# Performance work log

Measured on AMD Instinct MI355X. Metric: run time of the kernel, lower is better.

The kernel has to match this reference:

```python
import jax, jax.numpy as jnp
import numpy as np

N_TRUCK = 100000
N_CAR = 100000
E = 1600000
H = 128
P = 200000


def _gcn(x, edge_index, edge_weight, W, b, num_nodes):
    """PyG GCNConv: D^{-1/2}(A+I)D^{-1/2} x W + b with self-loop weight 1."""
    h = x @ W  # [N, H]
    row, col = edge_index[0], edge_index[1]
    deg = jax.ops.segment_sum(edge_weight, col, num_segments=num_nodes) + 1.0  # +1 self-loop
    dis = jax.lax.rsqrt(deg)
    norm = dis[row] * edge_weight * dis[col]  # [E]
    agg = jax.ops.segment_sum(norm[:, None] * h[row], col, num_segments=num_nodes)
    agg = agg + (dis * dis)[:, None] * h  # self-loop contribution
    return agg + b


def setup_inputs() -> dict:
    key = jax.random.key(0)
    ks = jax.random.split(key, 12)
    return {
        "x_car": jax.random.normal(ks[0], (N_CAR, 3), dtype=jnp.float32),
        "edge_index_truck": jax.random.randint(ks[1], (2, E), 0, N_TRUCK, dtype=jnp.int64)
        if jax.config.jax_enable_x64 else jax.random.randint(ks[1], (2, E), 0, N_TRUCK, dtype=jnp.int32),
        "edge_index_car": jax.random.randint(ks[2], (2, E), 0, N_CAR, dtype=jnp.int32),
        "edge_weight_car": jax.random.uniform(ks[3], (E,), dtype=jnp.float32),
        "src": jax.random.randint(ks[4], (P,), 0, N_TRUCK + N_CAR, dtype=jnp.int32),
        "dst": jax.random.randint(ks[5], (P,), 0, N_TRUCK + N_CAR, dtype=jnp.int32),
        "n_truck": N_TRUCK,
        "W_truck": jax.random.normal(ks[6], (1, H), dtype=jnp.float32) * 0.5,
        "b_truck": jax.random.normal(ks[7], (H,), dtype=jnp.float32) * 0.1,
        "W_car": jax.random.normal(ks[8], (3, H), dtype=jnp.float32) * 0.5,
        "b_car": jax.random.normal(ks[9], (H,), dtype=jnp.float32) * 0.1,
        "W_lin": jax.random.normal(ks[10], (H, 1), dtype=jnp.float32) * 0.1,
        "b_lin": jax.random.normal(ks[11], (1,), dtype=jnp.float32) * 0.1,
    }


def reference(x_car, edge_index_truck, edge_index_car, edge_weight_car,
              src, dst, n_truck, W_truck, b_truck, W_car, b_car, W_lin, b_lin):
    x_truck_in = jnp.ones((n_truck, 1), dtype=x_car.dtype)
    ew_truck = jnp.ones((edge_index_truck.shape[1],), dtype=x_car.dtype)
    h_truck = _gcn(x_truck_in, edge_index_truck, ew_truck, W_truck, b_truck, n_truck)
    h_car = _gcn(x_car, edge_index_car, edge_weight_car, W_car, b_car, x_car.shape[0])
    x = jnp.concatenate([h_truck, h_car], axis=0)  # [N_truck+N_car, H]
    score = (x[src] * x[dst]) @ W_lin + b_lin  # [P, 1]
    return score
```

## Files before the change

kernel.cpp:

```cpp
#include <hip/hip_runtime.h>

typedef unsigned long long u64;

#define N_TRUCK 100000
#define BLK 256
#define NB 256
#define NPB 391
#define CAP 8192
#define PB 512
#define BLK_P 1024
#define CHUNK_MAX 3136
#define ROW_MASK 0x1FFFFu
#define LC_SHIFT 17

#define WS_NEED_NEW 29569920ULL


__global__ void k_place(const int* __restrict__ trow, const int* __restrict__ tcol,
                        const int* __restrict__ crow, const int* __restrict__ ccol,
                        const float* __restrict__ ew, int E_,
                        int* __restrict__ curT, int* __restrict__ curC,
                        unsigned* __restrict__ pT, u64* __restrict__ pC8,
                        const float* __restrict__ Wt, const float* __restrict__ bt,
                        const float* __restrict__ Wc, const float* __restrict__ bc,
                        const float* __restrict__ wlin, float* __restrict__ G) {
    if (blockIdx.x == PB) {
        int l = threadIdx.x;
        if (l < 64) {
            float acc[21];
#pragma unroll
            for (int k = 0; k < 21; k++) acc[k] = 0.0f;
            for (int h = l; h < 128; h += 64) {
                float m[6] = {Wt[h], bt[h], Wc[h], Wc[128 + h], Wc[256 + h], bc[h]};
                float w = wlin[h];
                int k = 0;
#pragma unroll
                for (int a = 0; a < 6; a++)
#pragma unroll
                    for (int b2 = a; b2 < 6; b2++)
                        acc[k++] += m[a] * m[b2] * w;
            }
            int k = 0;
#pragma unroll
            for (int a = 0; a < 6; a++)
#pragma unroll
                for (int b2 = a; b2 < 6; b2++) {
                    float v = acc[k++];
#pragma unroll
                    for (int off = 32; off; off >>= 1) v += __shfl_down(v, off);
                    if (l == 0) {
                        G[a * 6 + b2] = v;
                        G[b2 * 6 + a] = v;
                    }
                }
        }
        return;
    }

    __shared__ u64 pay8[CHUNK_MAX];
    __shared__ unsigned char bkt[CHUNK_MAX];
    __shared__ int hist[NB];
    __shared__ int shiftA[NB];
    unsigned* pay4 = (unsigned*)pay8;

    int b = blockIdx.x;
    int chunk = (E_ + PB - 1) / PB;
    int s0 = b * chunk, s1 = min(E_, s0 + chunk);
    int n = s1 - s0;
    int t = threadIdx.x;

    for (int k = t; k < NB; k += BLK_P) hist[k] = 0;
    __syncthreads();
    for (int j = s0 + t; j < s1; j += BLK_P) atomicAdd(&hist[tcol[j] / NPB], 1);
    __syncthreads();
    int myCnt = (t < NB) ? hist[t] : 0;
    if (t < NB) shiftA[t] = myCnt;
    __syncthreads();
    for (int off = 1; off < NB; off <<= 1) {
        int x = (t < NB && t >= off) ? shiftA[t - off] : 0;
        __syncthreads();
        if (t < NB) shiftA[t] += x;
        __syncthreads();
    }
    if (t < NB) {
        int excl = shiftA[t] - myCnt;
        int gstart = t * CAP + atomicAdd(&curT[t], myCnt);
        shiftA[t] = gstart - excl;
        hist[t] = excl;
    }
    __syncthreads();
    for (int j = s0 + t; j < s1; j += BLK_P) {
        int tc = tcol[j];
        int k = tc / NPB;
        int s = atomicAdd(&hist[k], 1);
        pay4[s] = ((unsigned)(tc - k * NPB) << LC_SHIFT) | (unsigned)trow[j];
        bkt[s] = (unsigned char)k;
    }
    __syncthreads();
    for (int s = t; s < n; s += BLK_P)
        pT[s + shiftA[bkt[s]]] = pay4[s];
    __syncthreads();

    for (int k = t; k < NB; k += BLK_P) hist[k] = 0;
    __syncthreads();
    for (int j = s0 + t; j < s1; j += BLK_P) atomicAdd(&hist[ccol[j] / NPB], 1);
    __syncthreads();
    myCnt = (t < NB) ? hist[t] : 0;
    if (t < NB) shiftA[t] = myCnt;
    __syncthreads();
    for (int off = 1; off < NB; off <<= 1) {
        int x = (t < NB && t >= off) ? shiftA[t - off] : 0;
        __syncthreads();
        if (t < NB) shiftA[t] += x;
        __syncthreads();
    }
    if (t < NB) {
        int excl = shiftA[t] - myCnt;
        int gstart = t * CAP + atomicAdd(&curC[t], myCnt);
        shiftA[t] = gstart - excl;
        hist[t] = excl;
    }
    __syncthreads();
    for (int j = s0 + t; j < s1; j += BLK_P) {
        int cc = ccol[j];
        int k = cc / NPB;
        int s = atomicAdd(&hist[k], 1);
        unsigned lo = ((unsigned)(cc - k * NPB) << LC_SHIFT) | (unsigned)crow[j];
        pay8[s] = ((u64)__float_as_uint(ew[j]) << 32) | lo;
        bkt[s] = (unsigned char)k;
    }
    __syncthreads();
    for (int s = t; s < n; s += BLK_P)
        pC8[s + shiftA[bkt[s]]] = pay8[s];
}


__global__ void k_deg2(const unsigned* __restrict__ pT, const u64* __restrict__ pC8,
                       const int* __restrict__ curT, const int* __restrict__ curC,
                       const float* __restrict__ x_car,
                       float* __restrict__ dis_t, float* __restrict__ dis_c,
                       float4* __restrict__ xs4, int nt, int nc) {
    __shared__ float acc[NPB];
    int b = blockIdx.x;
    bool car = b >= NB;
    int bk = car ? b - NB : b;
    int cnt = car ? curC[bk] : curT[bk];
    int s0 = bk * CAP;
    for (int k = threadIdx.x; k < NPB; k += blockDim.x) acc[k] = 0.0f;
    __syncthreads();
    if (car) {
        const ulonglong2* p2 = (const ulonglong2*)(pC8 + s0);
        int half = cnt >> 1;
        for (int j = threadIdx.x; j < half; j += blockDim.x) {
            ulonglong2 v = p2[j];
            atomicAdd(&acc[((unsigned)v.x) >> LC_SHIFT], __uint_as_float((unsigned)(v.x >> 32)));
            atomicAdd(&acc[((unsigned)v.y) >> LC_SHIFT], __uint_as_float((unsigned)(v.y >> 32)));
        }
        if ((cnt & 1) && threadIdx.x == 0) {
            u64 v = pC8[s0 + cnt - 1];
            atomicAdd(&acc[((unsigned)v) >> LC_SHIFT], __uint_as_float((unsigned)(v >> 32)));
        }
    } else {
        const uint2* p2 = (const uint2*)(pT + s0);
        int half = cnt >> 1;
        for (int j = threadIdx.x; j < half; j += blockDim.x) {
            uint2 v = p2[j];
            atomicAdd(&acc[v.x >> LC_SHIFT], 1.0f);
            atomicAdd(&acc[v.y >> LC_SHIFT], 1.0f);
        }
        if ((cnt & 1) && threadIdx.x == 0)
            atomicAdd(&acc[pT[s0 + cnt - 1] >> LC_SHIFT], 1.0f);
    }
    __syncthreads();
    int ntot = car ? nc : nt;
    for (int nn = threadIdx.x; nn < NPB; nn += blockDim.x) {
        int node = bk * NPB + nn;
        if (node < ntot) {
            float d = rsqrtf(acc[nn] + 1.0f);
            if (car) {
                dis_c[node] = d;
                const float* xn = &x_car[3 * node];
                xs4[node] = make_float4(d * xn[0], d * xn[1], d * xn[2], d);
            } else {
                dis_t[node] = d;
            }
        }
    }
}


__global__ void k_agg(const unsigned* __restrict__ pT, const u64* __restrict__ pC8,
                      const int* __restrict__ curT, const int* __restrict__ curC,
                      const float* __restrict__ dis_t, const float* __restrict__ dis_c,
                      const float4* __restrict__ xs4,
                      float* __restrict__ s_t, float4* __restrict__ y4,
                      int nt, int nc) {
    int b = blockIdx.x;
    if (b < NB) {
        __shared__ float sacc[NPB];
        int cnt = curT[b];
        int s0 = b * CAP;
        for (int k = threadIdx.x; k < NPB; k += blockDim.x) sacc[k] = 0.0f;
        __syncthreads();
        const uint2* p2 = (const uint2*)(pT + s0);
        int half = cnt >> 1;
        for (int j = threadIdx.x; j < half; j += blockDim.x) {
            uint2 v = p2[j];
            float da = dis_t[v.x & ROW_MASK];
            float db = dis_t[v.y & ROW_MASK];
            atomicAdd(&sacc[v.x >> LC_SHIFT], da);
            atomicAdd(&sacc[v.y >> LC_SHIFT], db);
        }
        if ((cnt & 1) && threadIdx.x == 0) {
            unsigned v = pT[s0 + cnt - 1];
            atomicAdd(&sacc[v >> LC_SHIFT], dis_t[v & ROW_MASK]);
        }
        __syncthreads();
        for (int nn = threadIdx.x; nn < NPB; nn += blockDim.x) {
            int node = b * NPB + nn;
            if (node < nt) {
                float d = dis_t[node];
                s_t[node] = fmaf(d, sacc[nn], d * d);
            }
        }
    } else {
        int bk = b - NB;
        __shared__ float y[NPB * 5];
        __shared__ float dcl[NPB];
        int cnt = curC[bk];
        int s0 = bk * CAP;
        for (int k = threadIdx.x; k < NPB * 5; k += blockDim.x) y[k] = 0.0f;
        for (int k = threadIdx.x; k < NPB; k += blockDim.x) {
            int node = bk * NPB + k;
            dcl[k] = (node < nc) ? dis_c[node] : 0.0f;
        }
        __syncthreads();
        const ulonglong2* p2 = (const ulonglong2*)(pC8 + s0);
        int half = cnt >> 1;
        for (int j = threadIdx.x; j < half; j += blockDim.x) {
            ulonglong2 v = p2[j];
            unsigned loa = (unsigned)v.x, lob = (unsigned)v.y;
            float4 xa = xs4[loa & ROW_MASK];
            float4 xb = xs4[lob & ROW_MASK];
            int lca = loa >> LC_SHIFT, lcb = lob >> LC_SHIFT;
            float na = __uint_as_float((unsigned)(v.x >> 32)) * dcl[lca];
            float nb = __uint_as_float((unsigned)(v.y >> 32)) * dcl[lcb];
            atomicAdd(&y[lca * 5 + 0], na * xa.x);
            atomicAdd(&y[lca * 5 + 1], na * xa.y);
            atomicAdd(&y[lca * 5 + 2], na * xa.z);
            atomicAdd(&y[lcb * 5 + 0], nb * xb.x);
            atomicAdd(&y[lcb * 5 + 1], nb * xb.y);
            atomicAdd(&y[lcb * 5 + 2], nb * xb.z);
        }
        if ((cnt & 1) && threadIdx.x == 0) {
            u64 v = pC8[s0 + cnt - 1];
            unsigned lo = (unsigned)v;
            float4 xa = xs4[lo & ROW_MASK];
            int lc = lo >> LC_SHIFT;
            float na = __uint_as_float((unsigned)(v >> 32)) * dcl[lc];
            atomicAdd(&y[lc * 5 + 0], na * xa.x);
            atomicAdd(&y[lc * 5 + 1], na * xa.y);
            atomicAdd(&y[lc * 5 + 2], na * xa.z);
        }
        __syncthreads();
        for (int nn = threadIdx.x; nn < NPB; nn += blockDim.x) {
            int node = bk * NPB + nn;
            if (node < nc) {
                float d = dcl[nn];
                float4 xs = xs4[node];
                y4[node] = make_float4(fmaf(d, xs.x, y[nn * 5 + 0]),
                                       fmaf(d, xs.y, y[nn * 5 + 1]),
                                       fmaf(d, xs.z, y[nn * 5 + 2]), 1.0f);
            }
        }
    }
}


__device__ __forceinline__ void load_z(int i, const float* __restrict__ s_t,
                                       const float4* __restrict__ y4, float z[6]) {
    if (i < N_TRUCK) {
        z[0] = s_t[i]; z[1] = 1.0f; z[2] = 0.0f; z[3] = 0.0f; z[4] = 0.0f; z[5] = 0.0f;
    } else {
        float4 y = y4[i - N_TRUCK];
        z[0] = 0.0f; z[1] = 0.0f; z[2] = y.x; z[3] = y.y; z[4] = y.z; z[5] = 1.0f;
    }
}

__global__ void k_pairs(const int* __restrict__ src, const int* __restrict__ dst, int P_,
                        const float* __restrict__ s_t, const float4* __restrict__ y4,
                        const float* __restrict__ G, const float* __restrict__ b_lin,
                        float* __restrict__ out) {
    int p = blockIdx.x * blockDim.x + threadIdx.x;
    if (p >= P_) return;
    float zs[6], zd[6];
    load_z(src[p], s_t, y4, zs);
    load_z(dst[p], s_t, y4, zd);
    float acc = 0.0f;
#pragma unroll
    for (int a = 0; a < 6; a++) {
        float g = 0.0f;
#pragma unroll
        for (int b = 0; b < 6; b++) g = fmaf(G[a * 6 + b], zd[b], g);
        acc = fmaf(zs[a], g, acc);
    }
    out[p] = acc + b_lin[0];
}


__global__ void k_G(const float* __restrict__ Wt, const float* __restrict__ bt,
                    const float* __restrict__ Wc, const float* __restrict__ bc,
                    const float* __restrict__ wlin, float* __restrict__ G) {
    int l = threadIdx.x;
    float acc[21];
#pragma unroll
    for (int k = 0; k < 21; k++) acc[k] = 0.0f;
    for (int h = l; h < 128; h += 64) {
        float m[6] = {Wt[h], bt[h], Wc[h], Wc[128 + h], Wc[256 + h], bc[h]};
        float w = wlin[h];
        int k = 0;
#pragma unroll
        for (int a = 0; a < 6; a++)
#pragma unroll
            for (int b = a; b < 6; b++)
                acc[k++] += m[a] * m[b] * w;
    }
    int k = 0;
#pragma unroll
    for (int a = 0; a < 6; a++)
#pragma unroll
        for (int b = a; b < 6; b++) {
            float v = acc[k++];
#pragma unroll
            for (int off = 32; off; off >>= 1) v += __shfl_down(v, off);
            if (l == 0) {
                G[a * 6 + b] = v;
                G[b * 6 + a] = v;
            }
        }
}

__global__ void k_deg(const int* __restrict__ tcol, const int* __restrict__ ccol,
                      const float* __restrict__ ew, int E_,
                      int* __restrict__ cnt_t, float* __restrict__ degw_c) {
    int i = blockIdx.x * blockDim.x + threadIdx.x;
    if (i >= E_) return;
    atomicAdd(&cnt_t[tcol[i]], 1);
    atomicAdd(&degw_c[ccol[i]], ew[i]);
}

__global__ void k_dis(const int* __restrict__ cnt_t, const float* __restrict__ degw_c,
                      float* __restrict__ dis_t, float* __restrict__ dis_c,
                      int nt, int nc) {
    int i = blockIdx.x * blockDim.x + threadIdx.x;
    if (i < nt) dis_t[i] = rsqrtf((float)cnt_t[i] + 1.0f);
    if (i < nc) dis_c[i] = rsqrtf(degw_c[i] + 1.0f);
}

__global__ void k_scat(const int* __restrict__ trow, const int* __restrict__ tcol,
                       const int* __restrict__ crow, const int* __restrict__ ccol,
                       const float* __restrict__ ew, int E_,
                       const float* __restrict__ dis_t, const float* __restrict__ dis_c,
                       const float* __restrict__ x_car,
                       float* __restrict__ sumdis, float* __restrict__ y4) {
    int i = blockIdx.x * blockDim.x + threadIdx.x;
    if (i >= E_) return;
    atomicAdd(&sumdis[tcol[i]], dis_t[trow[i]]);
    int r = crow[i], c = ccol[i];
    float nrm = dis_c[r] * ew[i] * dis_c[c];
    atomicAdd(&y4[c * 4 + 0], nrm * x_car[r * 3 + 0]);
    atomicAdd(&y4[c * 4 + 1], nrm * x_car[r * 3 + 1]);
    atomicAdd(&y4[c * 4 + 2], nrm * x_car[r * 3 + 2]);
}

__global__ void k_fin(int nt, int nc,
                      const float* __restrict__ dis_t, const float* __restrict__ sumdis,
                      float* __restrict__ s_t,
                      const float* __restrict__ dis_c, const float* __restrict__ x_car,
                      float* __restrict__ y4) {
    int i = blockIdx.x * blockDim.x + threadIdx.x;
    if (i < nt) {
        float d = dis_t[i];
        s_t[i] = d * sumdis[i] + d * d;
    }
    if (i < nc) {
        float d2 = dis_c[i] * dis_c[i];
        y4[i * 4 + 0] += d2 * x_car[i * 3 + 0];
        y4[i * 4 + 1] += d2 * x_car[i * 3 + 1];
        y4[i * 4 + 2] += d2 * x_car[i * 3 + 2];
        y4[i * 4 + 3] = 1.0f;
    }
}


extern "C" void kernel_launch(void* const* d_in, const int* in_sizes, int n_in,
                              void* d_out, int out_size, void* d_ws, size_t ws_size,
                              hipStream_t stream) {
    const float* x_car  = (const float*)d_in[0];
    const int*   ei_t   = (const int*)d_in[1];
    const int*   ei_c   = (const int*)d_in[2];
    const float* ew_c   = (const float*)d_in[3];
    const int*   src    = (const int*)d_in[4];
    const int*   dst    = (const int*)d_in[5];
    const float* W_t    = (const float*)d_in[7];
    const float* b_t    = (const float*)d_in[8];
    const float* W_c    = (const float*)d_in[9];
    const float* b_c    = (const float*)d_in[10];
    const float* W_lin  = (const float*)d_in[11];
    const float* b_lin  = (const float*)d_in[12];
    float* out = (float*)d_out;

    const int NC = in_sizes[0] / 3;
    const int E_ = in_sizes[1] / 2;
    const int P_ = in_sizes[4];

    const int* trow = ei_t;  const int* tcol = ei_t + E_;
    const int* crow = ei_c;  const int* ccol = ei_c + E_;

    char* ws = (char*)d_ws;
    int gP = (P_ + BLK - 1) / BLK;
    int chunk = (E_ + PB - 1) / PB;

    if (ws_size >= WS_NEED_NEW && chunk <= CHUNK_MAX && NB * NPB >= N_TRUCK &&
        NB * NPB >= NC && NB * CAP >= E_ + 8192) {
        int*      curT  = (int*)(ws + 0);
        int*      curC  = (int*)(ws + 1024);
        float*    G     = (float*)(ws + 2048);
        float*    dis_t = (float*)(ws + 4096);
        float*    dis_c = (float*)(ws + 404096);
        float*    s_t   = (float*)(ws + 804096);
        float*    y4    = (float*)(ws + 1204096);
        float4*   xs4   = (float4*)(ws + 2804096);
        unsigned* pT    = (unsigned*)(ws + 4404096);
        u64*      pC8   = (u64*)(ws + 12792704);

        hipMemsetAsync(ws, 0, 2048, stream);
        k_place<<<PB + 1, BLK_P, 0, stream>>>(trow, tcol, crow, ccol, ew_c, E_,
                                              curT, curC, pT, pC8,
                                              W_t, b_t, W_c, b_c, W_lin, G);
        k_deg2<<<2 * NB, BLK_P, 0, stream>>>(pT, pC8, curT, curC, x_car,
                                             dis_t, dis_c, xs4, N_TRUCK, NC);
        k_agg<<<2 * NB, BLK_P, 0, stream>>>(pT, pC8, curT, curC, dis_t, dis_c,
                                            xs4, s_t, (float4*)y4, N_TRUCK, NC);
        k_pairs<<<gP, BLK, 0, stream>>>(src, dst, P_, s_t, (const float4*)y4, G, b_lin, out);
    } else {
        int*   cnt_t  = (int*)(ws + 0);
        float* sumdis = (float*)(ws + 400000);
        float* degw_c = (float*)(ws + 800000);
        float* y4     = (float*)(ws + 1200000);
        float* dis_t  = (float*)(ws + 2800000);
        float* dis_c  = (float*)(ws + 3200000);
        float* s_t    = (float*)(ws + 3600000);
        float* G      = (float*)(ws + 4000000);

        hipMemsetAsync(ws, 0, 2800000, stream);
        int gE = (E_ + BLK - 1) / BLK;
        int gN = ((N_TRUCK > NC ? N_TRUCK : NC) + BLK - 1) / BLK;
        k_deg<<<gE, BLK, 0, stream>>>(tcol, ccol, ew_c, E_, cnt_t, degw_c);
        k_dis<<<gN, BLK, 0, stream>>>(cnt_t, degw_c, dis_t, dis_c, N_TRUCK, NC);
        k_scat<<<gE, BLK, 0, stream>>>(trow, tcol, crow, ccol, ew_c, E_,
                                       dis_t, dis_c, x_car, sumdis, y4);
        k_fin<<<gN, BLK, 0, stream>>>(N_TRUCK, NC, dis_t, sumdis, s_t, dis_c, x_car, y4);
        k_G<<<1, 64, 0, stream>>>(W_t, b_t, W_c, b_c, W_lin, G);
        k_pairs<<<gP, BLK, 0, stream>>>(src, dst, P_, s_t, (const float4*)y4, G, b_lin, out);
    }
}
```

Baseline: 184.2 us.

## Fuse whole GCN pipeline into one cooperative kernel with grid syncs

Replaces the multi-kernel pipeline (memset, place, deg, agg, pairs) with a single cooperative kernel that uses grid.sync between phases. Placement now uses a deterministic per-block histogram followed by a global prefix scan instead of global atomic cursors, so it no longer needs a memset. The aim is to remove launch gaps and kernel boundaries. The costs are extra grid barriers, a second pass over the column arrays, and host-side occupancy queries on every call. It falls back to the old path if a cooperative launch isn't possible.

```diff
diff --git a/kernel.cpp b/kernel.cpp
--- a/kernel.cpp
+++ b/kernel.cpp
@@ -1,5 +1,7 @@
 #include <hip/hip_runtime.h>
-
+#include <hip/hip_cooperative_groups.h>
+
+namespace cg = cooperative_groups;
 typedef unsigned long long u64;
 
 #define N_TRUCK 100000
@@ -13,7 +15,389 @@
 #define ROW_MASK 0x1FFFFu
 #define LC_SHIFT 17
 
+#define WS_NEED_F 30618496ULL
 #define WS_NEED_NEW 29569920ULL
+
+struct FParams {
+    const int *trow, *tcol, *crow, *ccol;
+    const float* ew;
+    const int *src, *dst;
+    const float *Wt, *bt, *Wc, *bc, *wlin, *blin;
+    const float* x_car;
+    float* out;
+    int E, P, NC;
+    float* G;
+    int *totT, *totC, *cntT, *cntC;
+    float *dis_t, *dis_c, *s_t;
+    float4 *y4, *xs4;
+    unsigned* pT;
+    u64* pC8;
+};
+
+union SmemU {
+    struct { int hT[NB]; int hC[NB]; } hist;
+    struct { int w[16]; } scan;
+    struct {
+        u64 pay8[CHUNK_MAX];
+        unsigned char bkt[CHUNK_MAX];
+        int hist[NB];
+        int shift[NB];
+        int wsum[16];
+    } place;
+    struct { float acc[NPB]; } deg;
+    struct { float y[NPB * 5]; float dcl[NPB]; } agg;
+};
+
+__device__ __forceinline__ void load_zf(int i, const float* __restrict__ s_t,
+                                        const float4* __restrict__ y4, float z[6]) {
+    if (i < N_TRUCK) {
+        z[0] = s_t[i]; z[1] = 1.0f; z[2] = 0.0f; z[3] = 0.0f; z[4] = 0.0f; z[5] = 0.0f;
+    } else {
+        float4 y = y4[i - N_TRUCK];
+        z[0] = 0.0f; z[1] = 0.0f; z[2] = y.x; z[3] = y.y; z[4] = y.z; z[5] = 1.0f;
+    }
+}
+
+__global__ __launch_bounds__(1024, 8)
+void k_fused(FParams fp) {
+    cg::grid_group grid = cg::this_grid();
+    __shared__ SmemU sm;
+    const int t = threadIdx.x;
+    const int b = blockIdx.x;
+    const int lane = t & 63, wv = t >> 6;
+    const int chunk = (fp.E + PB - 1) / PB;
+    const int s0 = b * chunk, s1 = min(fp.E, s0 + chunk);
+    const int n = s1 - s0;
+
+    for (int k = t; k < NB; k += BLK_P) { sm.hist.hT[k] = 0; sm.hist.hC[k] = 0; }
+    __syncthreads();
+    for (int j = s0 + t; j < s1; j += BLK_P) {
+        atomicAdd(&sm.hist.hT[fp.tcol[j] / NPB], 1);
+        atomicAdd(&sm.hist.hC[fp.ccol[j] / NPB], 1);
+    }
+    __syncthreads();
+    for (int k = t; k < NB; k += BLK_P) {
+        fp.cntT[k * PB + b] = sm.hist.hT[k];
+        fp.cntC[k * PB + b] = sm.hist.hC[k];
+    }
+    grid.sync();
+
+    {
+        bool car = b >= NB;
+        int k = b & (NB - 1);
+        int* row = (car ? fp.cntC : fp.cntT) + k * PB;
+        int v = 0, inc = 0;
+        if (t < PB) {
+            v = row[t];
+            inc = v;
+#pragma unroll
+            for (int off = 1; off < 64; off <<= 1) {
+                int nv = __shfl_up(inc, off);
+                if (lane >= off) inc += nv;
+            }
+            if (lane == 63) sm.scan.w[wv] = inc;
+        } else if (b == 0 && wv == 8) {
+            float acc[21];
+#pragma unroll
+            for (int q = 0; q < 21; q++) acc[q] = 0.0f;
+            for (int h = lane; h < 128; h += 64) {
+                float m[6] = {fp.Wt[h], fp.bt[h], fp.Wc[h], fp.Wc[128 + h], fp.Wc[256 + h], fp.bc[h]};
+                float w = fp.wlin[h];
+                int q = 0;
+#pragma unroll
+                for (int a = 0; a < 6; a++)
+#pragma unroll
+                    for (int b2 = a; b2 < 6; b2++)
+                        acc[q++] += m[a] * m[b2] * w;
+            }
+            int q = 0;
+#pragma unroll
+            for (int a = 0; a < 6; a++)
+#pragma unroll
+                for (int b2 = a; b2 < 6; b2++) {
+                    float vv = acc[q++];
+#pragma unroll
+                    for (int off = 32; off; off >>= 1) vv += __shfl_down(vv, off);
+                    if (lane == 0) {
+                        fp.G[a * 6 + b2] = vv;
+                        fp.G[b2 * 6 + a] = vv;
+                    }
+                }
+        }
+        __syncthreads();
+        if (t < 8) {
+            int pv = sm.scan.w[t], pinc = pv;
+#pragma unroll
+            for (int off = 1; off < 8; off <<= 1) {
+                int nv = __shfl_up(pinc, off);
+                if (lane >= off) pinc += nv;
+            }
+            sm.scan.w[t] = pinc - pv;
+        }
+        __syncthreads();
+        if (t < PB) {
+            int excl = (inc - v) + sm.scan.w[wv];
+            row[t] = excl;
+            if (t == PB - 1) (car ? fp.totC : fp.totT)[k] = excl + v;
+        }
+    }
+    grid.sync();
+
+    {
+        int cntk = 0, gbase = 0, inc = 0;
+        if (t < NB) {
+            int e0 = fp.cntT[t * PB + b];
+            int e1 = (b == PB - 1) ? fp.totT[t] : fp.cntT[t * PB + b + 1];
+            cntk = e1 - e0;
+            gbase = t * CAP + e0;
+            inc = cntk;
+#pragma unroll
+            for (int off = 1; off < 64; off <<= 1) {
+                int nv = __shfl_up(inc, off);
+                if (lane >= off) inc += nv;
+            }
+            if (lane == 63) sm.place.wsum[wv] = inc;
+        }
+        __syncthreads();
+        if (t < 4) {
+            int pv = sm.place.wsum[t], pinc = pv;
+#pragma unroll
+            for (int off = 1; off < 4; off <<= 1) {
+                int nv = __shfl_up(pinc, off);
+                if (lane >= off) pinc += nv;
+            }
+            sm.place.wsum[t] = pinc - pv;
+        }
+        __syncthreads();
+        if (t < NB) {
+            int lexcl = (inc - cntk) + sm.place.wsum[wv];
+            sm.place.hist[t] = lexcl;
+            sm.place.shift[t] = gbase - lexcl;
+        }
+        __syncthreads();
+        unsigned* pay4 = (unsigned*)sm.place.pay8;
+        for (int j = s0 + t; j < s1; j += BLK_P) {
+            int c = fp.tcol[j];
+            int k = c / NPB;
+            int s = atomicAdd(&sm.place.hist[k], 1);
+            pay4[s] = ((unsigned)(c - k * NPB) << LC_SHIFT) | (unsigned)fp.trow[j];
+            sm.place.bkt[s] = (unsigned char)k;
+        }
+        __syncthreads();
+        for (int s = t; s < n; s += BLK_P)
+            fp.pT[s + sm.place.shift[sm.place.bkt[s]]] = pay4[s];
+        __syncthreads();
+    }
+    {
+        int cntk = 0, gbase = 0, inc = 0;
+        if (t < NB) {
+            int e0 = fp.cntC[t * PB + b];
+            int e1 = (b == PB - 1) ? fp.totC[t] : fp.cntC[t * PB + b + 1];
+            cntk = e1 - e0;
+            gbase = t * CAP + e0;
+            inc = cntk;
+#pragma unroll
+            for (int off = 1; off < 64; off <<= 1) {
+                int nv = __shfl_up(inc, off);
+                if (lane >= off) inc += nv;
+            }
+            if (lane == 63) sm.place.wsum[wv] = inc;
+        }
+        __syncthreads();
+        if (t < 4) {
+            int pv = sm.place.wsum[t], pinc = pv;
+#pragma unroll
+            for (int off = 1; off < 4; off <<= 1) {
+                int nv = __shfl_up(pinc, off);
+                if (lane >= off) pinc += nv;
+            }
+            sm.place.wsum[t] = pinc - pv;
+        }
+        __syncthreads();
+        if (t < NB) {
+            int lexcl = (inc - cntk) + sm.place.wsum[wv];
+            sm.place.hist[t] = lexcl;
+            sm.place.shift[t] = gbase - lexcl;
+        }
+        __syncthreads();
+        for (int j = s0 + t; j < s1; j += BLK_P) {
+            int c = fp.ccol[j];
+            int k = c / NPB;
+            int s = atomicAdd(&sm.place.hist[k], 1);
+            unsigned lo = ((unsigned)(c - k * NPB) << LC_SHIFT) | (unsigned)fp.crow[j];
+            sm.place.pay8[s] = ((u64)__float_as_uint(fp.ew[j]) << 32) | lo;
+            sm.place.bkt[s] = (unsigned char)k;
+        }
+        __syncthreads();
+        for (int s = t; s < n; s += BLK_P)
+            fp.pC8[s + sm.place.shift[sm.place.bkt[s]]] = sm.place.pay8[s];
+    }
+    grid.sync();
+
+    {
+        bool car = b >= NB;
+        int bk = car ? b - NB : b;
+        int cnt = car ? fp.totC[bk] : fp.totT[bk];
+        int base = bk * CAP;
+        for (int k = t; k < NPB; k += BLK_P) sm.deg.acc[k] = 0.0f;
+        __syncthreads();
+        if (car) {
+            const ulonglong4* p4 = (const ulonglong4*)(fp.pC8 + base);
+            int q = cnt >> 2;
+            for (int j = t; j < q; j += BLK_P) {
+                ulonglong4 v = p4[j];
+                atomicAdd(&sm.deg.acc[((unsigned)v.x) >> LC_SHIFT], __uint_as_float((unsigned)(v.x >> 32)));
+                atomicAdd(&sm.deg.acc[((unsigned)v.y) >> LC_SHIFT], __uint_as_float((unsigned)(v.y >> 32)));
+                atomicAdd(&sm.deg.acc[((unsigned)v.z) >> LC_SHIFT], __uint_as_float((unsigned)(v.z >> 32)));
+                atomicAdd(&sm.deg.acc[((unsigned)v.w) >> LC_SHIFT], __uint_as_float((unsigned)(v.w >> 32)));
+            }
+            for (int j = (q << 2) + t; j < cnt; j += BLK_P) {
+                u64 v = fp.pC8[base + j];
+                atomicAdd(&sm.deg.acc[((unsigned)v) >> LC_SHIFT], __uint_as_float((unsigned)(v >> 32)));
+            }
+        } else {
+            const uint4* p4 = (const uint4*)(fp.pT + base);
+            int q = cnt >> 2;
+            for (int j = t; j < q; j += BLK_P) {
+                uint4 v = p4[j];
+                atomicAdd(&sm.deg.acc[v.x >> LC_SHIFT], 1.0f);
+                atomicAdd(&sm.deg.acc[v.y >> LC_SHIFT], 1.0f);
+                atomicAdd(&sm.deg.acc[v.z >> LC_SHIFT], 1.0f);
+                atomicAdd(&sm.deg.acc[v.w >> LC_SHIFT], 1.0f);
+            }
+            for (int j = (q << 2) + t; j < cnt; j += BLK_P)
+                atomicAdd(&sm.deg.acc[fp.pT[base + j] >> LC_SHIFT], 1.0f);
+        }
+        __syncthreads();
+        int ntot = car ? fp.NC : N_TRUCK;
+        for (int nn = t; nn < NPB; nn += BLK_P) {
+            int node = bk * NPB + nn;
+            if (node < ntot) {
+                float d = rsqrtf(sm.deg.acc[nn] + 1.0f);
+                if (car) {
+                    fp.dis_c[node] = d;
+                    const float* xn = &fp.x_car[3 * node];
+                    fp.xs4[node] = make_float4(d * xn[0], d * xn[1], d * xn[2], d);
+                } else {
+                    fp.dis_t[node] = d;
+                }
+            }
+        }
+    }
+    grid.sync();
+
+    if (b < NB) {
+        int cnt = fp.totT[b];
+        int base = b * CAP;
+        for (int k = t; k < NPB; k += BLK_P) sm.deg.acc[k] = 0.0f;
+        __syncthreads();
+        const uint4* p4 = (const uint4*)(fp.pT + base);
+        int q = cnt >> 2;
+        for (int j = t; j < q; j += BLK_P) {
+            uint4 v = p4[j];
+            float d0 = fp.dis_t[v.x & ROW_MASK];
+            float d1 = fp.dis_t[v.y & ROW_MASK];
+            float d2 = fp.dis_t[v.z & ROW_MASK];
+            float d3 = fp.dis_t[v.w & ROW_MASK];
+            atomicAdd(&sm.deg.acc[v.x >> LC_SHIFT], d0);
+            atomicAdd(&sm.deg.acc[v.y >> LC_SHIFT], d1);
+            atomicAdd(&sm.deg.acc[v.z >> LC_SHIFT], d2);
+            atomicAdd(&sm.deg.acc[v.w >> LC_SHIFT], d3);
+        }
+        for (int j = (q << 2) + t; j < cnt; j += BLK_P) {
+            unsigned v = fp.pT[base + j];
+            atomicAdd(&sm.deg.acc[v >> LC_SHIFT], fp.dis_t[v & ROW_MASK]);
+        }
+        __syncthreads();
+        for (int nn = t; nn < NPB; nn += BLK_P) {
+            int node = b * NPB + nn;
+            if (node < N_TRUCK) {
+                float d = fp.dis_t[node];
+                fp.s_t[node] = fmaf(d, sm.deg.acc[nn], d * d);
+            }
+        }
+    } else {
+        int bk = b - NB;
+        int cnt = fp.totC[bk];
+        int base = bk * CAP;
+        for (int k = t; k < NPB * 5; k += BLK_P) sm.agg.y[k] = 0.0f;
+        for (int k = t; k < NPB; k += BLK_P) {
+            int node = bk * NPB + k;
+            sm.agg.dcl[k] = (node < fp.NC) ? fp.dis_c[node] : 0.0f;
+        }
+        __syncthreads();
+        const ulonglong4* p4 = (const ulonglong4*)(fp.pC8 + base);
+        int q = cnt >> 2;
+        for (int j = t; j < q; j += BLK_P) {
+            ulonglong4 v = p4[j];
+            unsigned lo0 = (unsigned)v.x, lo1 = (unsigned)v.y;
+            unsigned lo2 = (unsigned)v.z, lo3 = (unsigned)v.w;
+            float4 x0 = fp.xs4[lo0 & ROW_MASK];
+            float4 x1 = fp.xs4[lo1 & ROW_MASK];
+            float4 x2 = fp.xs4[lo2 & ROW_MASK];
+            float4 x3 = fp.xs4[lo3 & ROW_MASK];
+            int c0 = lo0 >> LC_SHIFT, c1 = lo1 >> LC_SHIFT;
+            int c2 = lo2 >> LC_SHIFT, c3 = lo3 >> LC_SHIFT;
+            float n0 = __uint_as_float((unsigned)(v.x >> 32)) * sm.agg.dcl[c0];
+            float n1 = __uint_as_float((unsigned)(v.y >> 32)) * sm.agg.dcl[c1];
+            float n2 = __uint_as_float((unsigned)(v.z >> 32)) * sm.agg.dcl[c2];
+            float n3 = __uint_as_float((unsigned)(v.w >> 32)) * sm.agg.dcl[c3];
+            atomicAdd(&sm.agg.y[c0 * 5 + 0], n0 * x0.x);
+            atomicAdd(&sm.agg.y[c0 * 5 + 1], n0 * x0.y);
+            atomicAdd(&sm.agg.y[c0 * 5 + 2], n0 * x0.z);
+            atomicAdd(&sm.agg.y[c1 * 5 + 0], n1 * x1.x);
+            atomicAdd(&sm.agg.y[c1 * 5 + 1], n1 * x1.y);
+            atomicAdd(&sm.agg.y[c1 * 5 + 2], n1 * x1.z);
+            atomicAdd(&sm.agg.y[c2 * 5 + 0], n2 * x2.x);
+            atomicAdd(&sm.agg.y[c2 * 5 + 1], n2 * x2.y);
+            atomicAdd(&sm.agg.y[c2 * 5 + 2], n2 * x2.z);
+            atomicAdd(&sm.agg.y[c3 * 5 + 0], n3 * x3.x);
+            atomicAdd(&sm.agg.y[c3 * 5 + 1], n3 * x3.y);
+            atomicAdd(&sm.agg.y[c3 * 5 + 2], n3 * x3.z);
+        }
+        for (int j = (q << 2) + t; j < cnt; j += BLK_P) {
+            u64 v = fp.pC8[base + j];
+            unsigned lo = (unsigned)v;
+            float4 xa = fp.xs4[lo & ROW_MASK];
+            int lc = lo >> LC_SHIFT;
+            float na = __uint_as_float((unsigned)(v >> 32)) * sm.agg.dcl[lc];
+            atomicAdd(&sm.agg.y[lc * 5 + 0], na * xa.x);
+            atomicAdd(&sm.agg.y[lc * 5 + 1], na * xa.y);
+            atomicAdd(&sm.agg.y[lc * 5 + 2], na * xa.z);
+        }
+        __syncthreads();
+        for (int nn = t; nn < NPB; nn += BLK_P) {
+            int node = bk * NPB + nn;
+            if (node < fp.NC) {
+                float d = sm.agg.dcl[nn];
+                float4 xs = fp.xs4[node];
+                fp.y4[node] = make_float4(fmaf(d, xs.x, sm.agg.y[nn * 5 + 0]),
+                                          fmaf(d, xs.y, sm.agg.y[nn * 5 + 1]),
+                                          fmaf(d, xs.z, sm.agg.y[nn * 5 + 2]), 1.0f);
+            }
+        }
+    }
+    grid.sync();
+
+    float Gl[36];
+#pragma unroll
+    for (int k = 0; k < 36; k++) Gl[k] = fp.G[k];
+    float bl = fp.blin[0];
+    for (int p = b * BLK_P + t; p < fp.P; p += gridDim.x * BLK_P) {
+        float zs[6], zd[6];
+        load_zf(fp.src[p], fp.s_t, fp.y4, zs);
+        load_zf(fp.dst[p], fp.s_t, fp.y4, zd);
+        float acc = 0.0f;
+#pragma unroll
+        for (int a = 0; a < 6; a++) {
+            float g = 0.0f;
+#pragma unroll
+            for (int b2 = 0; b2 < 6; b2++) g = fmaf(Gl[a * 6 + b2], zd[b2], g);
+            acc = fmaf(zs[a], g, acc);
+        }
+        fp.out[p] = acc + bl;
+    }
+}
 
 
 __global__ void k_place(const int* __restrict__ trow, const int* __restrict__ tcol,
@@ -134,7 +518,6 @@
         pC8[s + shiftA[bkt[s]]] = pay8[s];
 }
 
-
 __global__ void k_deg2(const unsigned* __restrict__ pT, const u64* __restrict__ pC8,
                        const int* __restrict__ curT, const int* __restrict__ curC,
                        const float* __restrict__ x_car,
@@ -187,7 +570,6 @@
         }
     }
 }
-
 
 __global__ void k_agg(const unsigned* __restrict__ pT, const u64* __restrict__ pC8,
                       const int* __restrict__ curT, const int* __restrict__ curC,
@@ -276,17 +658,6 @@
     }
 }
 
-
-__device__ __forceinline__ void load_z(int i, const float* __restrict__ s_t,
-                                       const float4* __restrict__ y4, float z[6]) {
-    if (i < N_TRUCK) {
-        z[0] = s_t[i]; z[1] = 1.0f; z[2] = 0.0f; z[3] = 0.0f; z[4] = 0.0f; z[5] = 0.0f;
-    } else {
-        float4 y = y4[i - N_TRUCK];
-        z[0] = 0.0f; z[1] = 0.0f; z[2] = y.x; z[3] = y.y; z[4] = y.z; z[5] = 1.0f;
-    }
-}
-
 __global__ void k_pairs(const int* __restrict__ src, const int* __restrict__ dst, int P_,
                         const float* __restrict__ s_t, const float4* __restrict__ y4,
                         const float* __restrict__ G, const float* __restrict__ b_lin,
@@ -294,8 +665,8 @@
     int p = blockIdx.x * blockDim.x + threadIdx.x;
     if (p >= P_) return;
     float zs[6], zd[6];
-    load_z(src[p], s_t, y4, zs);
-    load_z(dst[p], s_t, y4, zd);
+    load_zf(src[p], s_t, y4, zs);
+    load_zf(dst[p], s_t, y4, zd);
     float acc = 0.0f;
 #pragma unroll
     for (int a = 0; a < 6; a++) {
@@ -420,6 +791,43 @@
     char* ws = (char*)d_ws;
     int gP = (P_ + BLK - 1) / BLK;
     int chunk = (E_ + PB - 1) / PB;
+
+    bool fused_ok = false;
+    if (ws_size >= WS_NEED_F && chunk <= CHUNK_MAX && NB * NPB >= N_TRUCK &&
+        NB * NPB >= NC && NC <= 131072 && NB * CAP >= E_ + CAP) {
+        int dev = 0, coop = 0, nblk = 0, cus = 0;
+        if (hipGetDevice(&dev) == hipSuccess &&
+            hipDeviceGetAttribute(&coop, hipDeviceAttributeCooperativeLaunch, dev) == hipSuccess &&
+            coop &&
+            hipOccupancyMaxActiveBlocksPerMultiprocessor(&nblk, (const void*)k_fused, BLK_P, 0) == hipSuccess &&
+            hipDeviceGetAttribute(&cus, hipDeviceAttributeMultiprocessorCount, dev) == hipSuccess &&
+            nblk * cus >= PB) {
+            FParams fpar;
+            fpar.trow = trow; fpar.tcol = tcol; fpar.crow = crow; fpar.ccol = ccol;
+            fpar.ew = ew_c; fpar.src = src; fpar.dst = dst;
+            fpar.Wt = W_t; fpar.bt = b_t; fpar.Wc = W_c; fpar.bc = b_c;
+            fpar.wlin = W_lin; fpar.blin = b_lin;
+            fpar.x_car = x_car; fpar.out = out;
+            fpar.E = E_; fpar.P = P_; fpar.NC = NC;
+            fpar.G     = (float*)(ws + 0);
+            fpar.totT  = (int*)(ws + 256);
+            fpar.totC  = (int*)(ws + 1280);
+            fpar.cntT  = (int*)(ws + 4096);
+            fpar.cntC  = (int*)(ws + 528384);
+            fpar.dis_t = (float*)(ws + 1052672);
+            fpar.dis_c = (float*)(ws + 1452672);
+            fpar.s_t   = (float*)(ws + 1852672);
+            fpar.y4    = (float4*)(ws + 2252672);
+            fpar.xs4   = (float4*)(ws + 3852672);
+            fpar.pT    = (unsigned*)(ws + 5452672);
+            fpar.pC8   = (u64*)(ws + 13841280);
+            void* args[] = {(void*)&fpar};
+            if (hipLaunchCooperativeKernel((const void*)k_fused, dim3(PB), dim3(BLK_P),
+                                           args, 0, stream) == hipSuccess)
+                fused_ok = true;
+        }
+    }
+    if (fused_ok) return;
 
     if (ws_size >= WS_NEED_NEW && chunk <= CHUNK_MAX && NB * NPB >= N_TRUCK &&
         NB * NPB >= NC && NB * CAP >= E_ + 8192) {
```

Measured after the change: 185.3 us. About the same (+0.6%).

## Restructure edge bucketing with wave-shuffle scans, fused histograms, smaller blocks, wider loads

Applied to the files above, without the earlier changes.

The bucketing kernel is relaunched with twice as many half-size blocks. It computes the truck and car histograms in one pass over the edges and replaces the barrier-heavy shared-memory prefix scan with a wave-level shuffle scan. The degree and aggregation kernels now load four packed edges per thread instead of two, and launch bounds are added to all three kernels. The aim is fewer barriers, better occupancy and fewer memory instructions, at the cost of twice as many global atomics on the bucket cursors and more register use.

```diff
diff --git a/kernel.cpp b/kernel.cpp
--- a/kernel.cpp
+++ b/kernel.cpp
@@ -7,23 +7,25 @@
 #define NB 256
 #define NPB 391
 #define CAP 8192
-#define PB 512
+#define PB 1024
+#define BLK_PL 512
 #define BLK_P 1024
-#define CHUNK_MAX 3136
+#define CHUNK_MAX 1568
 #define ROW_MASK 0x1FFFFu
 #define LC_SHIFT 17
 
 #define WS_NEED_NEW 29569920ULL
 
 
-__global__ void k_place(const int* __restrict__ trow, const int* __restrict__ tcol,
-                        const int* __restrict__ crow, const int* __restrict__ ccol,
-                        const float* __restrict__ ew, int E_,
-                        int* __restrict__ curT, int* __restrict__ curC,
-                        unsigned* __restrict__ pT, u64* __restrict__ pC8,
-                        const float* __restrict__ Wt, const float* __restrict__ bt,
-                        const float* __restrict__ Wc, const float* __restrict__ bc,
-                        const float* __restrict__ wlin, float* __restrict__ G) {
+__global__ __launch_bounds__(BLK_PL, 8)
+void k_place(const int* __restrict__ trow, const int* __restrict__ tcol,
+             const int* __restrict__ crow, const int* __restrict__ ccol,
+             const float* __restrict__ ew, int E_,
+             int* __restrict__ curT, int* __restrict__ curC,
+             unsigned* __restrict__ pT, u64* __restrict__ pC8,
+             const float* __restrict__ Wt, const float* __restrict__ bt,
+             const float* __restrict__ Wc, const float* __restrict__ bc,
+             const float* __restrict__ wlin, float* __restrict__ G) {
     if (blockIdx.x == PB) {
         int l = threadIdx.x;
         if (l < 64) {
@@ -59,121 +61,160 @@
 
     __shared__ u64 pay8[CHUNK_MAX];
     __shared__ unsigned char bkt[CHUNK_MAX];
-    __shared__ int hist[NB];
+    __shared__ int hT[NB], hC[NB];
     __shared__ int shiftA[NB];
+    __shared__ int wsum[8];
     unsigned* pay4 = (unsigned*)pay8;
 
-    int b = blockIdx.x;
-    int chunk = (E_ + PB - 1) / PB;
-    int s0 = b * chunk, s1 = min(E_, s0 + chunk);
-    int n = s1 - s0;
-    int t = threadIdx.x;
-
-    for (int k = t; k < NB; k += BLK_P) hist[k] = 0;
+    const int b = blockIdx.x;
+    const int t = threadIdx.x;
+    const int lane = t & 63, wv = t >> 6;
+    const int chunk = (E_ + PB - 1) / PB;
+    const int s0 = b * chunk, s1 = min(E_, s0 + chunk);
+    const int n = s1 - s0;
+
+    for (int k = t; k < NB; k += BLK_PL) { hT[k] = 0; hC[k] = 0; }
     __syncthreads();
-    for (int j = s0 + t; j < s1; j += BLK_P) atomicAdd(&hist[tcol[j] / NPB], 1);
+    for (int j = s0 + t; j < s1; j += BLK_PL) {
+        int tc = tcol[j];
+        int cc = ccol[j];
+        atomicAdd(&hT[tc / NPB], 1);
+        atomicAdd(&hC[cc / NPB], 1);
+    }
     __syncthreads();
-    int myCnt = (t < NB) ? hist[t] : 0;
-    if (t < NB) shiftA[t] = myCnt;
-    __syncthreads();
-    for (int off = 1; off < NB; off <<= 1) {
-        int x = (t < NB && t >= off) ? shiftA[t - off] : 0;
-        __syncthreads();
-        if (t < NB) shiftA[t] += x;
-        __syncthreads();
-    }
-    if (t < NB) {
-        int excl = shiftA[t] - myCnt;
-        int gstart = t * CAP + atomicAdd(&curT[t], myCnt);
-        shiftA[t] = gstart - excl;
-        hist[t] = excl;
-    }
-    __syncthreads();
-    for (int j = s0 + t; j < s1; j += BLK_P) {
-        int tc = tcol[j];
-        int k = tc / NPB;
-        int s = atomicAdd(&hist[k], 1);
-        pay4[s] = ((unsigned)(tc - k * NPB) << LC_SHIFT) | (unsigned)trow[j];
-        bkt[s] = (unsigned char)k;
-    }
-    __syncthreads();
-    for (int s = t; s < n; s += BLK_P)
-        pT[s + shiftA[bkt[s]]] = pay4[s];
-    __syncthreads();
-
-    for (int k = t; k < NB; k += BLK_P) hist[k] = 0;
-    __syncthreads();
-    for (int j = s0 + t; j < s1; j += BLK_P) atomicAdd(&hist[ccol[j] / NPB], 1);
-    __syncthreads();
-    myCnt = (t < NB) ? hist[t] : 0;
-    if (t < NB) shiftA[t] = myCnt;
-    __syncthreads();
-    for (int off = 1; off < NB; off <<= 1) {
-        int x = (t < NB && t >= off) ? shiftA[t - off] : 0;
-        __syncthreads();
-        if (t < NB) shiftA[t] += x;
-        __syncthreads();
-    }
-    if (t < NB) {
-        int excl = shiftA[t] - myCnt;
-        int gstart = t * CAP + atomicAdd(&curC[t], myCnt);
-        shiftA[t] = gstart - excl;
-        hist[t] = excl;
-    }
-    __syncthreads();
-    for (int j = s0 + t; j < s1; j += BLK_P) {
-        int cc = ccol[j];
-        int k = cc / NPB;
-        int s = atomicAdd(&hist[k], 1);
-        unsigned lo = ((unsigned)(cc - k * NPB) << LC_SHIFT) | (unsigned)crow[j];
-        pay8[s] = ((u64)__float_as_uint(ew[j]) << 32) | lo;
-        bkt[s] = (unsigned char)k;
-    }
-    __syncthreads();
-    for (int s = t; s < n; s += BLK_P)
-        pC8[s + shiftA[bkt[s]]] = pay8[s];
-}
-
-
-__global__ void k_deg2(const unsigned* __restrict__ pT, const u64* __restrict__ pC8,
-                       const int* __restrict__ curT, const int* __restrict__ curC,
-                       const float* __restrict__ x_car,
-                       float* __restrict__ dis_t, float* __restrict__ dis_c,
-                       float4* __restrict__ xs4, int nt, int nc) {
+
+    {
+        int cntk = 0, inc = 0;
+        if (t < NB) {
+            cntk = hT[t];
+            inc = cntk;
+#pragma unroll
+            for (int off = 1; off < 64; off <<= 1) {
+                int nv = __shfl_up(inc, off);
+                if (lane >= off) inc += nv;
+            }
+            if (lane == 63) wsum[wv] = inc;
+        }
+        __syncthreads();
+        if (t < 4) {
+            int pv = wsum[t], pinc = pv;
+#pragma unroll
+            for (int off = 1; off < 4; off <<= 1) {
+                int nv = __shfl_up(pinc, off);
+                if (lane >= off) pinc += nv;
+            }
+            wsum[t] = pinc - pv;
+        }
+        __syncthreads();
+        if (t < NB) {
+            int lexcl = (inc - cntk) + wsum[wv];
+            int gstart = t * CAP + atomicAdd(&curT[t], cntk);
+            hT[t] = lexcl;
+            shiftA[t] = gstart - lexcl;
+        }
+        __syncthreads();
+        for (int j = s0 + t; j < s1; j += BLK_PL) {
+            int tc = tcol[j];
+            int k = tc / NPB;
+            int s = atomicAdd(&hT[k], 1);
+            pay4[s] = ((unsigned)(tc - k * NPB) << LC_SHIFT) | (unsigned)trow[j];
+            bkt[s] = (unsigned char)k;
+        }
+        __syncthreads();
+        for (int s = t; s < n; s += BLK_PL)
+            pT[s + shiftA[bkt[s]]] = pay4[s];
+        __syncthreads();
+    }
+
+    {
+        int cntk = 0, inc = 0;
+        if (t < NB) {
+            cntk = hC[t];
+            inc = cntk;
+#pragma unroll
+            for (int off = 1; off < 64; off <<= 1) {
+                int nv = __shfl_up(inc, off);
+                if (lane >= off) inc += nv;
+            }
+            if (lane == 63) wsum[wv] = inc;
+        }
+        __syncthreads();
+        if (t < 4) {
+            int pv = wsum[t], pinc = pv;
+#pragma unroll
+            for (int off = 1; off < 4; off <<= 1) {
+                int nv = __shfl_up(pinc, off);
+                if (lane >= off) pinc += nv;
+            }
+            wsum[t] = pinc - pv;
+        }
+        __syncthreads();
+        if (t < NB) {
+            int lexcl = (inc - cntk) + wsum[wv];
+            int gstart = t * CAP + atomicAdd(&curC[t], cntk);
+            hC[t] = lexcl;
+            shiftA[t] = gstart - lexcl;
+        }
+        __syncthreads();
+        for (int j = s0 + t; j < s1; j += BLK_PL) {
+            int cc = ccol[j];
+            int k = cc / NPB;
+            int s = atomicAdd(&hC[k], 1);
+            unsigned lo = ((unsigned)(cc - k * NPB) << LC_SHIFT) | (unsigned)crow[j];
+            pay8[s] = ((u64)__float_as_uint(ew[j]) << 32) | lo;
+            bkt[s] = (unsigned char)k;
+        }
+        __syncthreads();
+        for (int s = t; s < n; s += BLK_PL)
+            pC8[s + shiftA[bkt[s]]] = pay8[s];
+    }
+}
+
+
+__global__ __launch_bounds__(BLK_P, 8)
+void k_deg2(const unsigned* __restrict__ pT, const u64* __restrict__ pC8,
+            const int* __restrict__ curT, const int* __restrict__ curC,
+            const float* __restrict__ x_car,
+            float* __restrict__ dis_t, float* __restrict__ dis_c,
+            float4* __restrict__ xs4, int nt, int nc) {
     __shared__ float acc[NPB];
     int b = blockIdx.x;
     bool car = b >= NB;
     int bk = car ? b - NB : b;
     int cnt = car ? curC[bk] : curT[bk];
-    int s0 = bk * CAP;
-    for (int k = threadIdx.x; k < NPB; k += blockDim.x) acc[k] = 0.0f;
+    int base = bk * CAP;
+    for (int k = threadIdx.x; k < NPB; k += BLK_P) acc[k] = 0.0f;
     __syncthreads();
     if (car) {
-        const ulonglong2* p2 = (const ulonglong2*)(pC8 + s0);
-        int half = cnt >> 1;
-        for (int j = threadIdx.x; j < half; j += blockDim.x) {
-            ulonglong2 v = p2[j];
+        const ulonglong4* p4 = (const ulonglong4*)(pC8 + base);
+        int q = cnt >> 2;
+        for (int j = threadIdx.x; j < q; j += BLK_P) {
+            ulonglong4 v = p4[j];
             atomicAdd(&acc[((unsigned)v.x) >> LC_SHIFT], __uint_as_float((unsigned)(v.x >> 32)));
             atomicAdd(&acc[((unsigned)v.y) >> LC_SHIFT], __uint_as_float((unsigned)(v.y >> 32)));
-        }
-        if ((cnt & 1) && threadIdx.x == 0) {
-            u64 v = pC8[s0 + cnt - 1];
+            atomicAdd(&acc[((unsigned)v.z) >> LC_SHIFT], __uint_as_float((unsigned)(v.z >> 32)));
+            atomicAdd(&acc[((unsigned)v.w) >> LC_SHIFT], __uint_as_float((unsigned)(v.w >> 32)));
+        }
+        for (int j = (q << 2) + threadIdx.x; j < cnt; j += BLK_P) {
+            u64 v = pC8[base + j];
             atomicAdd(&acc[((unsigned)v) >> LC_SHIFT], __uint_as_float((unsigned)(v >> 32)));
         }
     } else {
-        const uint2* p2 = (const uint2*)(pT + s0);
-        int half = cnt >> 1;
-        for (int j = threadIdx.x; j < half; j += blockDim.x) {
-            uint2 v = p2[j];
+        const uint4* p4 = (const uint4*)(pT + base);
+        int q = cnt >> 2;
+        for (int j = threadIdx.x; j < q; j += BLK_P) {
+            uint4 v = p4[j];
             atomicAdd(&acc[v.x >> LC_SHIFT], 1.0f);
             atomicAdd(&acc[v.y >> LC_SHIFT], 1.0f);
-        }
-        if ((cnt & 1) && threadIdx.x == 0)
-            atomicAdd(&acc[pT[s0 + cnt - 1] >> LC_SHIFT], 1.0f);
+            atomicAdd(&acc[v.z >> LC_SHIFT], 1.0f);
+            atomicAdd(&acc[v.w >> LC_SHIFT], 1.0f);
+        }
+        for (int j = (q << 2) + threadIdx.x; j < cnt; j += BLK_P)
+            atomicAdd(&acc[pT[base + j] >> LC_SHIFT], 1.0f);
     }
     __syncthreads();
     int ntot = car ? nc : nt;
-    for (int nn = threadIdx.x; nn < NPB; nn += blockDim.x) {
+    for (int nn = threadIdx.x; nn < NPB; nn += BLK_P) {
         int node = bk * NPB + nn;
         if (node < ntot) {
             float d = rsqrtf(acc[nn] + 1.0f);
@@ -189,34 +230,39 @@
 }
 
 
-__global__ void k_agg(const unsigned* __restrict__ pT, const u64* __restrict__ pC8,
-                      const int* __restrict__ curT, const int* __restrict__ curC,
-                      const float* __restrict__ dis_t, const float* __restrict__ dis_c,
-                      const float4* __restrict__ xs4,
-                      float* __restrict__ s_t, float4* __restrict__ y4,
-                      int nt, int nc) {
+__global__ __launch_bounds__(BLK_P, 8)
+void k_agg(const unsigned* __restrict__ pT, const u64* __restrict__ pC8,
+           const int* __restrict__ curT, const int* __restrict__ curC,
+           const float* __restrict__ dis_t, const float* __restrict__ dis_c,
+           const float4* __restrict__ xs4,
+           float* __restrict__ s_t, float4* __restrict__ y4,
+           int nt, int nc) {
     int b = blockIdx.x;
     if (b < NB) {
         __shared__ float sacc[NPB];
         int cnt = curT[b];
-        int s0 = b * CAP;
-        for (int k = threadIdx.x; k < NPB; k += blockDim.x) sacc[k] = 0.0f;
-        __syncthreads();
-        const uint2* p2 = (const uint2*)(pT + s0);
-        int half = cnt >> 1;
-        for (int j = threadIdx.x; j < half; j += blockDim.x) {
-            uint2 v = p2[j];
-            float da = dis_t[v.x & ROW_MASK];
-            float db = dis_t[v.y & ROW_MASK];
-            atomicAdd(&sacc[v.x >> LC_SHIFT], da);
-            atomicAdd(&sacc[v.y >> LC_SHIFT], db);
-        }
-        if ((cnt & 1) && threadIdx.x == 0) {
-            unsigned v = pT[s0 + cnt - 1];
+        int base = b * CAP;
+        for (int k = threadIdx.x; k < NPB; k += BLK_P) sacc[k] = 0.0f;
+        __syncthreads();
+        const uint4* p4 = (const uint4*)(pT + base);
+        int q = cnt >> 2;
+        for (int j = threadIdx.x; j < q; j += BLK_P) {
+            uint4 v = p4[j];
+            float d0 = dis_t[v.x & ROW_MASK];
+            float d1 = dis_t[v.y & ROW_MASK];
+            float d2 = dis_t[v.z & ROW_MASK];
+            float d3 = dis_t[v.w & ROW_MASK];
+            atomicAdd(&sacc[v.x >> LC_SHIFT], d0);
+            atomicAdd(&sacc[v.y >> LC_SHIFT], d1);
+            atomicAdd(&sacc[v.z >> LC_SHIFT], d2);
+            atomicAdd(&sacc[v.w >> LC_SHIFT], d3);
+        }
+        for (int j = (q << 2) + threadIdx.x; j < cnt; j += BLK_P) {
+            unsigned v = pT[base + j];
             atomicAdd(&sacc[v >> LC_SHIFT], dis_t[v & ROW_MASK]);
         }
         __syncthreads();
-        for (int nn = threadIdx.x; nn < NPB; nn += blockDim.x) {
+        for (int nn = threadIdx.x; nn < NPB; nn += BLK_P) {
             int node = b * NPB + nn;
             if (node < nt) {
                 float d = dis_t[node];
@@ -228,32 +274,44 @@
         __shared__ float y[NPB * 5];
         __shared__ float dcl[NPB];
         int cnt = curC[bk];
-        int s0 = bk * CAP;
-        for (int k = threadIdx.x; k < NPB * 5; k += blockDim.x) y[k] = 0.0f;
-        for (int k = threadIdx.x; k < NPB; k += blockDim.x) {
+        int base = bk * CAP;
+        for (int k = threadIdx.x; k < NPB * 5; k += BLK_P) y[k] = 0.0f;
+        for (int k = threadIdx.x; k < NPB; k += BLK_P) {
             int node = bk * NPB + k;
             dcl[k] = (node < nc) ? dis_c[node] : 0.0f;
         }
         __syncthreads();
-        const ulonglong2* p2 = (const ulonglong2*)(pC8 + s0);
-        int half = cnt >> 1;
-        for (int j = threadIdx.x; j < half; j += blockDim.x) {
-            ulonglong2 v = p2[j];
-            unsigned loa = (unsigned)v.x, lob = (unsigned)v.y;
-            float4 xa = xs4[loa & ROW_MASK];
-            float4 xb = xs4[lob & ROW_MASK];
-            int lca = loa >> LC_SHIFT, lcb = lob >> LC_SHIFT;
-            float na = __uint_as_float((unsigned)(v.x >> 32)) * dcl[lca];
-            float nb = __uint_as_float((unsigned)(v.y >> 32)) * dcl[lcb];
-            atomicAdd(&y[lca * 5 + 0], na * xa.x);
-            atomicAdd(&y[lca * 5 + 1], na * xa.y);
-            atomicAdd(&y[lca * 5 + 2], na * xa.z);
-            atomicAdd(&y[lcb * 5 + 0], nb * xb.x);
-            atomicAdd(&y[lcb * 5 + 1], nb * xb.y);
-            atomicAdd(&y[lcb * 5 + 2], nb * xb.z);
-        }
-        if ((cnt & 1) && threadIdx.x == 0) {
-            u64 v = pC8[s0 + cnt - 1];
+        const ulonglong4* p4 = (const ulonglong4*)(pC8 + base);
+        int q = cnt >> 2;
+        for (int j = threadIdx.x; j < q; j += BLK_P) {
+            ulonglong4 v = p4[j];
+            unsigned lo0 = (unsigned)v.x, lo1 = (unsigned)v.y;
+            unsigned lo2 = (unsigned)v.z, lo3 = (unsigned)v.w;
+            float4 x0 = xs4[lo0 & ROW_MASK];
+            float4 x1 = xs4[lo1 & ROW_MASK];
+            float4 x2 = xs4[lo2 & ROW_MASK];
+            float4 x3 = xs4[lo3 & ROW_MASK];
+            int c0 = lo0 >> LC_SHIFT, c1 = lo1 >> LC_SHIFT;
+            int c2 = lo2 >> LC_SHIFT, c3 = lo3 >> LC_SHIFT;
+            float n0 = __uint_as_float((unsigned)(v.x >> 32)) * dcl[c0];
+            float n1 = __uint_as_float((unsigned)(v.y >> 32)) * dcl[c1];
+            float n2 = __uint_as_float((unsigned)(v.z >> 32)) * dcl[c2];
+            float n3 = __uint_as_float((unsigned)(v.w >> 32)) * dcl[c3];
+            atomicAdd(&y[c0 * 5 + 0], n0 * x0.x);
+            atomicAdd(&y[c0 * 5 + 1], n0 * x0.y);
+            atomicAdd(&y[c0 * 5 + 2], n0 * x0.z);
+            atomicAdd(&y[c1 * 5 + 0], n1 * x1.x);
+            atomicAdd(&y[c1 * 5 + 1], n1 * x1.y);
+            atomicAdd(&y[c1 * 5 + 2], n1 * x1.z);
+            atomicAdd(&y[c2 * 5 + 0], n2 * x2.x);
+            atomicAdd(&y[c2 * 5 + 1], n2 * x2.y);
+            atomicAdd(&y[c2 * 5 + 2], n2 * x2.z);
+            atomicAdd(&y[c3 * 5 + 0], n3 * x3.x);
+            atomicAdd(&y[c3 * 5 + 1], n3 * x3.y);
+            atomicAdd(&y[c3 * 5 + 2], n3 * x3.z);
+        }
+        for (int j = (q << 2) + threadIdx.x; j < cnt; j += BLK_P) {
+            u64 v = pC8[base + j];
             unsigned lo = (unsigned)v;
             float4 xa = xs4[lo & ROW_MASK];
             int lc = lo >> LC_SHIFT;
@@ -263,7 +321,7 @@
             atomicAdd(&y[lc * 5 + 2], na * xa.z);
         }
         __syncthreads();
-        for (int nn = threadIdx.x; nn < NPB; nn += blockDim.x) {
+        for (int nn = threadIdx.x; nn < NPB; nn += BLK_P) {
             int node = bk * NPB + nn;
             if (node < nc) {
                 float d = dcl[nn];
@@ -277,8 +335,8 @@
 }
 
 
-__device__ __forceinline__ void load_z(int i, const float* __restrict__ s_t,
-                                       const float4* __restrict__ y4, float z[6]) {
+__device__ __forceinline__ void load_zf(int i, const float* __restrict__ s_t,
+                                        const float4* __restrict__ y4, float z[6]) {
     if (i < N_TRUCK) {
         z[0] = s_t[i]; z[1] = 1.0f; z[2] = 0.0f; z[3] = 0.0f; z[4] = 0.0f; z[5] = 0.0f;
     } else {
@@ -294,8 +352,8 @@
     int p = blockIdx.x * blockDim.x + threadIdx.x;
     if (p >= P_) return;
     float zs[6], zd[6];
-    load_z(src[p], s_t, y4, zs);
-    load_z(dst[p], s_t, y4, zd);
+    load_zf(src[p], s_t, y4, zs);
+    load_zf(dst[p], s_t, y4, zd);
     float acc = 0.0f;
 #pragma unroll
     for (int a = 0; a < 6; a++) {
@@ -435,9 +493,9 @@
         u64*      pC8   = (u64*)(ws + 12792704);
 
         hipMemsetAsync(ws, 0, 2048, stream);
-        k_place<<<PB + 1, BLK_P, 0, stream>>>(trow, tcol, crow, ccol, ew_c, E_,
-                                              curT, curC, pT, pC8,
-                                              W_t, b_t, W_c, b_c, W_lin, G);
+        k_place<<<PB + 1, BLK_PL, 0, stream>>>(trow, tcol, crow, ccol, ew_c, E_,
+                                               curT, curC, pT, pC8,
+                                               W_t, b_t, W_c, b_c, W_lin, G);
         k_deg2<<<2 * NB, BLK_P, 0, stream>>>(pT, pC8, curT, curC, x_car,
                                              dis_t, dis_c, xs4, N_TRUCK, NC);
         k_agg<<<2 * NB, BLK_P, 0, stream>>>(pT, pC8, curT, curC, dis_t, dis_c,
```

Measured after the change: 201.2 us. +9.2%, slower.
